# Kernel optimization log

Measured on AMD Instinct MI355X. Metric: run time of the kernel, lower is better.

The kernel has to match this reference:

```python
import jax, jax.numpy as jnp
import numpy as np

TOKENS = 512
IN_F = 8192
OUT_F = 8192
RANK = 64
NNZ = 8192
QMAX = 127.0  # int8 symmetric


def setup_inputs() -> dict:
    key = jax.random.key(0)
    ks = jax.random.split(key, 12)
    x = jax.random.normal(ks[0], (TOKENS, IN_F), dtype=jnp.float32)
    quantized_weight = jax.random.randint(ks[1], (OUT_F, IN_F), -128, 128, dtype=jnp.int32)
    weight_scale = jax.random.uniform(ks[2], (OUT_F,), minval=0.005, maxval=0.02, dtype=jnp.float32)
    smooth_scales = jax.random.uniform(ks[3], (IN_F,), minval=0.5, maxval=2.0, dtype=jnp.float32)
    act_scale = jnp.array([0.05], dtype=jnp.float32)
    outlier_rows = jax.random.randint(ks[4], (NNZ,), 0, OUT_F, dtype=jnp.int32)
    outlier_cols = jax.random.randint(ks[5], (NNZ,), 0, IN_F, dtype=jnp.int32)
    outlier_vals = jax.random.normal(ks[6], (NNZ,), dtype=jnp.float32) * 0.1
    svd_U = jax.random.normal(ks[7], (OUT_F, RANK), dtype=jnp.float32) * 0.02
    svd_S = jax.random.uniform(ks[8], (RANK,), minval=0.1, maxval=1.0, dtype=jnp.float32)
    svd_V = jax.random.normal(ks[9], (IN_F, RANK), dtype=jnp.float32) * 0.02
    bias = jax.random.normal(ks[10], (OUT_F,), dtype=jnp.float32) * 0.01
    return {"x": x, "quantized_weight": quantized_weight, "weight_scale": weight_scale,
            "smooth_scales": smooth_scales, "act_scale": act_scale,
            "outlier_rows": outlier_rows, "outlier_cols": outlier_cols,
            "outlier_vals": outlier_vals, "svd_U": svd_U, "svd_S": svd_S,
            "svd_V": svd_V, "bias": bias}


def reference(x, quantized_weight, weight_scale, smooth_scales, act_scale,
              outlier_rows, outlier_cols, outlier_vals, svd_U, svd_S, svd_V, bias):
    # SmoothQuant: migrate activation outliers into the weight scales
    x_s = x / smooth_scales  # [T, in]
    # per-tensor symmetric int8 activation fake-quant
    a = act_scale[0]
    x_q = jnp.clip(jnp.round(x_s / a), -QMAX - 1.0, QMAX)
    x_dq = x_q * a  # [T, in]
    # dequantize weight: per-output-channel scale, plus sparse outlier correction
    W = quantized_weight.astype(jnp.float32) * weight_scale[:, None]  # [out, in]
    W = W.at[outlier_rows, outlier_cols].add(outlier_vals)
    # dense quantized matmul
    y = x_dq @ W.T  # [T, out]
    # low-rank SVD residual: x @ (U S V^T)^T = ((x @ V) * S) @ U^T
    y = y + ((x_dq @ svd_V) * svd_S) @ svd_U.T
    return y + bias
```

## Files before the change

### kernel.cpp

```cpp
#include <hip/hip_runtime.h>
#include <hip/hip_bf16.h>

#define TOKENS 512
#define IN_F 8192
#define OUT_F 8192
#define RANK 64
#define NNZ 8192

#define KSPLIT 4
#define KRANGE (IN_F / KSPLIT)
#define BM 512
#define BN 64
#define BK 64
#define NT (KRANGE / BK)
#define LRSPLIT 16

typedef __attribute__((ext_vector_type(8))) short short8;
typedef __attribute__((ext_vector_type(4))) float f32x4;
typedef __attribute__((ext_vector_type(4))) int int4v;

__device__ __forceinline__ unsigned short f2bf(float f) {
  unsigned int u = __builtin_bit_cast(unsigned int, f);
  u += 0x7FFFu + ((u >> 16) & 1u);
  return (unsigned short)(u >> 16);
}
__device__ __forceinline__ float bf2f(unsigned short b) {
  unsigned int u = ((unsigned int)b) << 16;
  return __builtin_bit_cast(float, u);
}

__device__ __forceinline__ void gload_lds16(const void* g, void* l) {
  __builtin_amdgcn_global_load_lds(
      (const __attribute__((address_space(1))) unsigned int*)(g),
      (__attribute__((address_space(3))) unsigned int*)(l), 16, 0, 0);
}

#define WAIT_VM(n) asm volatile("s_waitcnt vmcnt(" #n ")" ::: "memory")
#define WAIT_LGKM0 asm volatile("s_waitcnt lgkmcnt(0)" ::: "memory")
#define SCHED0 __builtin_amdgcn_sched_barrier(0)

__global__ __launch_bounds__(256) void k_quant(const float* __restrict__ x,
                                               const float* __restrict__ smooth,
                                               const float* __restrict__ act,
                                               unsigned short* __restrict__ Abf,
                                               unsigned char* __restrict__ Aq) {
  int idx = blockIdx.x * 256 + threadIdx.x;
  int base = idx * 4;
  int col = base & (IN_F - 1);
  float a = act[0];
  float4 xx = *(const float4*)(x + base);
  float4 ss = *(const float4*)(smooth + col);
  float q0 = fminf(fmaxf(rintf((xx.x / ss.x) / a), -128.f), 127.f);
  float q1 = fminf(fmaxf(rintf((xx.y / ss.y) / a), -128.f), 127.f);
  float q2 = fminf(fmaxf(rintf((xx.z / ss.z) / a), -128.f), 127.f);
  float q3 = fminf(fmaxf(rintf((xx.w / ss.w) / a), -128.f), 127.f);
  ushort4 o;
  o.x = f2bf(q0); o.y = f2bf(q1); o.z = f2bf(q2); o.w = f2bf(q3);
  *(ushort4*)(Abf + base) = o;
  int i0 = (int)q0, i1 = (int)q1, i2 = (int)q2, i3 = (int)q3;
  unsigned int p = (i0 & 0xFF) | ((i1 & 0xFF) << 8) | ((i2 & 0xFF) << 16) |
                   ((unsigned)(i3 & 0xFF) << 24);
  *(unsigned int*)(Aq + base) = p;
}

__global__ __launch_bounds__(256) void k_lr1(const unsigned short* __restrict__ Abf,
                                             const float* __restrict__ V,
                                             const float* __restrict__ S,
                                             const float* __restrict__ act,
                                             float* __restrict__ t) {
  int bid = blockIdx.x;
  int mb = (bid & 3) * 128;
  int ksp = bid >> 2;
  int kb0 = ksp * 512;
  int tid = threadIdx.x, w = tid >> 6, l = tid & 63;
  int lr = l & 15, lg = l >> 4;
  f32x4 acc[2][4] = {};
  for (int ks = 0; ks < 16; ++ks) {
    int kb = kb0 + ks * 32;
    short8 af[2];
#pragma unroll
    for (int fi = 0; fi < 2; ++fi) {
      int row = mb + w * 32 + fi * 16 + lr;
      af[fi] = *(const short8*)(Abf + (size_t)row * IN_F + kb + lg * 8);
    }
    short8 bfr[4];
#pragma unroll
    for (int fj = 0; fj < 4; ++fj) {
      int rk = fj * 16 + lr;
      short8 bv;
#pragma unroll
      for (int j = 0; j < 8; ++j)
        bv[j] = (short)f2bf(V[(size_t)(kb + lg * 8 + j) * RANK + rk]);
      bfr[fj] = bv;
    }
#pragma unroll
    for (int fi = 0; fi < 2; ++fi)
#pragma unroll
      for (int fj = 0; fj < 4; ++fj)
        acc[fi][fj] = __builtin_amdgcn_mfma_f32_16x16x32_bf16(af[fi], bfr[fj], acc[fi][fj], 0, 0, 0);
  }
  float a = act[0];
  float* tk = t + (size_t)ksp * TOKENS * RANK;
#pragma unroll
  for (int fi = 0; fi < 2; ++fi)
#pragma unroll
    for (int fj = 0; fj < 4; ++fj) {
      int rk = fj * 16 + lr;
      float sc = a * S[rk];
#pragma unroll
      for (int r = 0; r < 4; ++r) {
        int tok = mb + w * 32 + fi * 16 + lg * 4 + r;
        tk[(size_t)tok * RANK + rk] = acc[fi][fj][r] * sc;
      }
    }
}

__global__ __launch_bounds__(256) void k_lr2(const float* __restrict__ t,
                                             const float* __restrict__ U,
                                             const float* __restrict__ bias,
                                             float* __restrict__ out) {
  int bid = blockIdx.x;
  int mb = (bid & 3) * 128;
  int nb = (bid >> 2) * 128;
  int tid = threadIdx.x, w = tid >> 6, l = tid & 63;
  int lr = l & 15, lg = l >> 4;
  int wm = w >> 1, wn = w & 1;
  f32x4 acc[4][4] = {};
#pragma unroll
  for (int kk = 0; kk < 2; ++kk) {
    short8 af[4], bfr[4];
#pragma unroll
    for (int fi = 0; fi < 4; ++fi) {
      int row = mb + wm * 64 + fi * 16 + lr;
      size_t off = (size_t)row * RANK + kk * 32 + lg * 8;
      float4 t0 = {0, 0, 0, 0}, t1 = {0, 0, 0, 0};
      for (int s = 0; s < LRSPLIT; ++s) {
        const float4* tp = (const float4*)(t + (size_t)s * TOKENS * RANK + off);
        float4 u0 = tp[0], u1 = tp[1];
        t0.x += u0.x; t0.y += u0.y; t0.z += u0.z; t0.w += u0.w;
        t1.x += u1.x; t1.y += u1.y; t1.z += u1.z; t1.w += u1.w;
      }
      af[fi][0] = f2bf(t0.x); af[fi][1] = f2bf(t0.y);
      af[fi][2] = f2bf(t0.z); af[fi][3] = f2bf(t0.w);
      af[fi][4] = f2bf(t1.x); af[fi][5] = f2bf(t1.y);
      af[fi][6] = f2bf(t1.z); af[fi][7] = f2bf(t1.w);
    }
#pragma unroll
    for (int fj = 0; fj < 4; ++fj) {
      int row = nb + wn * 64 + fj * 16 + lr;
      const float4* up = (const float4*)(U + (size_t)row * RANK + kk * 32 + lg * 8);
      float4 u0 = up[0], u1 = up[1];
      bfr[fj][0] = f2bf(u0.x); bfr[fj][1] = f2bf(u0.y);
      bfr[fj][2] = f2bf(u0.z); bfr[fj][3] = f2bf(u0.w);
      bfr[fj][4] = f2bf(u1.x); bfr[fj][5] = f2bf(u1.y);
      bfr[fj][6] = f2bf(u1.z); bfr[fj][7] = f2bf(u1.w);
    }
#pragma unroll
    for (int fi = 0; fi < 4; ++fi)
#pragma unroll
      for (int fj = 0; fj < 4; ++fj)
        acc[fi][fj] = __builtin_amdgcn_mfma_f32_16x16x32_bf16(af[fi], bfr[fj], acc[fi][fj], 0, 0, 0);
  }
#pragma unroll
  for (int fj = 0; fj < 4; ++fj) {
    int o = nb + wn * 64 + fj * 16 + lr;
    float b = bias[o];
#pragma unroll
    for (int fi = 0; fi < 4; ++fi)
#pragma unroll
      for (int r = 0; r < 4; ++r) {
        int tok = mb + wm * 64 + fi * 16 + lg * 4 + r;
        out[(size_t)tok * OUT_F + o] = b + acc[fi][fj][r];
      }
  }
}

__global__ __launch_bounds__(256) void k_outlier_merge(
    const unsigned short* __restrict__ Abf, const int* __restrict__ rows,
    const int* __restrict__ cols, const float* __restrict__ vals,
    const float* __restrict__ act, const float* __restrict__ wscale,
    const int* __restrict__ part, float* __restrict__ out) {
  __shared__ float accr[OUT_F];
  int tk = blockIdx.x;
  for (int i = threadIdx.x; i < OUT_F; i += 256) accr[i] = 0.f;
  __syncthreads();
  float a = act[0];
  for (int i = threadIdx.x; i < NNZ; i += 256) {
    int r = rows[i], c = cols[i];
    float v = vals[i];
    float xq = bf2f(Abf[(size_t)tk * IN_F + c]);
    atomicAdd(accr + r, a * xq * v);
  }
  __syncthreads();
  float* orow = out + (size_t)tk * OUT_F;
  const int* p0 = part + (size_t)tk * OUT_F;
  const int* p1 = p0 + (size_t)TOKENS * OUT_F;
  const int* p2 = p1 + (size_t)TOKENS * OUT_F;
  const int* p3 = p2 + (size_t)TOKENS * OUT_F;
  for (int i = threadIdx.x * 4; i < OUT_F; i += 1024) {
    int4v s0 = *(const int4v*)(p0 + i);
    int4v s1 = *(const int4v*)(p1 + i);
    int4v s2 = *(const int4v*)(p2 + i);
    int4v s3 = *(const int4v*)(p3 + i);
    float4 ws = *(const float4*)(wscale + i);
    float4 ov = *(const float4*)(orow + i);
    ov.x += accr[i + 0] + (float)(s0[0] + s1[0] + s2[0] + s3[0]) * a * ws.x;
    ov.y += accr[i + 1] + (float)(s0[1] + s1[1] + s2[1] + s3[1]) * a * ws.y;
    ov.z += accr[i + 2] + (float)(s0[2] + s1[2] + s2[2] + s3[2]) * a * ws.z;
    ov.w += accr[i + 3] + (float)(s0[3] + s1[3] + s2[3] + s3[3]) * a * ws.w;
    *(float4*)(orow + i) = ov;
  }
}

__global__ __launch_bounds__(512, 4) void k_gemm(const unsigned char* __restrict__ Aq,
                                                 const int* __restrict__ W,
                                                 int* __restrict__ part) {
  __shared__ __align__(16) unsigned char As[2][BM * BK];
  __shared__ __align__(16) unsigned char Bs[2][BN * BK];

  int d = blockIdx.x;
  int wg = (d & 7) * 64 + (d >> 3);
  int ks = wg >> 7;
  int nb = wg & 127;
  int kb0 = ks * KRANGE;

  int tid = threadIdx.x, w = tid >> 6, l = tid & 63;
  int lr = l & 15, lg = l >> 4;
  int wm = w >> 1, wn = w & 1;

  int4v acc[8][2] = {};
  int4v wa[2], wb[2];

  const int rW = tid >> 3;
  const int kcW = (tid & 7) * 8;
  const int uW = (kcW >> 4) ^ ((rW >> 1) & 3);
  const int offW = kcW & 15;

  auto LOAD_W = [&](int4v (&wr)[2], int kt) {
    const int* wp = W + (size_t)(nb * BN + rW) * IN_F + kb0 +
                    (kt & (NT - 1)) * BK + kcW;
    wr[0] = *(const int4v*)wp;
    wr[1] = *(const int4v*)(wp + 4);
  };
  auto STAGE_A = [&](int buf, int kt) {
    int kb = kb0 + (kt & (NT - 1)) * BK;
#pragma unroll
    for (int i = 0; i < 4; ++i) {
      int lidx = i * 512 + w * 64;
      int U = lidx + l;
      int r = U >> 2, up = U & 3;
      int u = up ^ ((r >> 1) & 3);
      gload_lds16(Aq + (size_t)r * IN_F + kb + u * 16, &As[buf][(size_t)lidx * 16]);
    }
  };
  auto DSWRITE_B = [&](int buf, const int4v (&wr)[2]) {
    unsigned int w0 = 0, w1 = 0;
#pragma unroll
    for (int j = 0; j < 4; ++j) w0 |= ((unsigned)(wr[0][j] & 0xFF)) << (8 * j);
#pragma unroll
    for (int j = 0; j < 4; ++j) w1 |= ((unsigned)(wr[1][j] & 0xFF)) << (8 * j);
    uint2 val; val.x = w0; val.y = w1;
    *(uint2*)(&Bs[buf][(size_t)rW * BK + uW * 16 + offW]) = val;
  };
  auto LDFA = [&](int buf, int row) -> int4v {
    int u = lg ^ ((row >> 1) & 3);
    return *(const int4v*)(&As[buf][(size_t)row * BK + u * 16]);
  };
  auto LDFB = [&](int buf, int row) -> int4v {
    int u = lg ^ ((row >> 1) & 3);
    return *(const int4v*)(&Bs[buf][(size_t)row * BK + u * 16]);
  };
  auto COMPUTE = [&](int buf) {
    int4v b0 = LDFB(buf, wn * 32 + lr);
    int4v b1 = LDFB(buf, wn * 32 + 16 + lr);
    __builtin_amdgcn_s_setprio(1);
#pragma unroll
    for (int fi = 0; fi < 8; ++fi) {
      int4v af = LDFA(buf, wm * 128 + fi * 16 + lr);
      acc[fi][0] = __builtin_amdgcn_mfma_i32_16x16x64_i8(af, b0, acc[fi][0], 0, 0, 0);
      acc[fi][1] = __builtin_amdgcn_mfma_i32_16x16x64_i8(af, b1, acc[fi][1], 0, 0, 0);
    }
    __builtin_amdgcn_s_setprio(0);
  };

  LOAD_W(wa, 0);
  STAGE_A(0, 0);
  WAIT_VM(4);
  DSWRITE_B(0, wa);
  LOAD_W(wa, 1);
  WAIT_VM(2);
  WAIT_LGKM0;
  SCHED0;
  __builtin_amdgcn_s_barrier();
  SCHED0;

#define ITER(kt, CUR, wcur, wnxt)                                   \
  {                                                                 \
    STAGE_A(CUR ^ 1, (kt) + 1);                                     \
    LOAD_W(wnxt, (kt) + 2);                                         \
    COMPUTE(CUR);                                                   \
    WAIT_VM(2);                                                     \
    DSWRITE_B(CUR ^ 1, wcur);                                       \
    WAIT_LGKM0;                                                     \
    SCHED0;                                                         \
    __builtin_amdgcn_s_barrier();                                   \
    SCHED0;                                                         \
  }

  for (int kt = 0; kt < NT; kt += 2) {
    ITER(kt, 0, wa, wb);
    ITER(kt + 1, 1, wb, wa);
  }
#undef ITER

  int* pp = part + (size_t)ks * TOKENS * OUT_F;
#pragma unroll
  for (int fj = 0; fj < 2; ++fj) {
    int o = nb * BN + wn * 32 + fj * 16 + lr;
#pragma unroll
    for (int fi = 0; fi < 8; ++fi)
#pragma unroll
      for (int rr = 0; rr < 4; ++rr) {
        int tok = wm * 128 + fi * 16 + lg * 4 + rr;
        pp[(size_t)tok * OUT_F + o] = acc[fi][fj][rr];
      }
  }
}

extern "C" void kernel_launch(void* const* d_in, const int* in_sizes, int n_in,
                              void* d_out, int out_size, void* d_ws, size_t ws_size,
                              hipStream_t stream) {
  const float* x = (const float*)d_in[0];
  const int* W = (const int*)d_in[1];
  const float* wscale = (const float*)d_in[2];
  const float* smooth = (const float*)d_in[3];
  const float* act = (const float*)d_in[4];
  const int* orow = (const int*)d_in[5];
  const int* ocol = (const int*)d_in[6];
  const float* oval = (const float*)d_in[7];
  const float* U = (const float*)d_in[8];
  const float* S = (const float*)d_in[9];
  const float* V = (const float*)d_in[10];
  const float* bias = (const float*)d_in[11];
  float* out = (float*)d_out;

  unsigned short* Abf = (unsigned short*)d_ws;
  unsigned char* Aq = (unsigned char*)d_ws + (size_t)TOKENS * IN_F * 2;
  float* t = (float*)((char*)d_ws + (size_t)TOKENS * IN_F * 3);
  int* part = (int*)((char*)d_ws + (size_t)TOKENS * IN_F * 3 +
                     (size_t)LRSPLIT * TOKENS * RANK * 4);

  k_quant<<<(TOKENS * IN_F / 4) / 256, 256, 0, stream>>>(x, smooth, act, Abf, Aq);
  k_gemm<<<512, 512, 0, stream>>>(Aq, W, part);
  k_lr1<<<64, 256, 0, stream>>>(Abf, V, S, act, t);
  k_lr2<<<256, 256, 0, stream>>>(t, U, bias, out);
  k_outlier_merge<<<TOKENS, 256, 0, stream>>>(Abf, orow, ocol, oval, act,
                                              wscale, part, out);
}
```

Baseline: 208.9 us.

## Rework int8 GEMM to 4 waves, BK=32, 16x16x32 MFMA, simpler pipeline

The int8 GEMM kernel now runs with 256 threads (4 waves) instead of 512. Each wave covers 128 token rows and all 64 output columns, using 8x4 accumulators. The K tile drops from 64 to 32 and the kernel switches to the 16x16x32 i8 MFMA with 8-byte LDS fragments. The hand-scheduled double-buffer macro is replaced by a plain loop with __syncthreads, and the explicit lgkm waits and sched barriers are removed. This trades fewer waves and more barriers per K for more register reuse of B fragments, which risks lower latency hiding and a slower MFMA variant.

```diff
diff --git a/kernel.cpp b/kernel.cpp
--- a/kernel.cpp
+++ b/kernel.cpp
@@ -11,7 +11,7 @@
 #define KRANGE (IN_F / KSPLIT)
 #define BM 512
 #define BN 64
-#define BK 64
+#define BK 32
 #define NT (KRANGE / BK)
 #define LRSPLIT 16
 
@@ -36,8 +36,6 @@
 }
 
 #define WAIT_VM(n) asm volatile("s_waitcnt vmcnt(" #n ")" ::: "memory")
-#define WAIT_LGKM0 asm volatile("s_waitcnt lgkmcnt(0)" ::: "memory")
-#define SCHED0 __builtin_amdgcn_sched_barrier(0)
 
 __global__ __launch_bounds__(256) void k_quant(const float* __restrict__ x,
                                                const float* __restrict__ smooth,
@@ -212,7 +210,7 @@
   }
 }
 
-__global__ __launch_bounds__(512, 4) void k_gemm(const unsigned char* __restrict__ Aq,
+__global__ __launch_bounds__(256, 3) void k_gemm(const unsigned char* __restrict__ Aq,
                                                  const int* __restrict__ W,
                                                  int* __restrict__ part) {
   __shared__ __align__(16) unsigned char As[2][BM * BK];
@@ -226,102 +224,94 @@
 
   int tid = threadIdx.x, w = tid >> 6, l = tid & 63;
   int lr = l & 15, lg = l >> 4;
-  int wm = w >> 1, wn = w & 1;
-
-  int4v acc[8][2] = {};
-  int4v wa[2], wb[2];
-
-  const int rW = tid >> 3;
-  const int kcW = (tid & 7) * 8;
-  const int uW = (kcW >> 4) ^ ((rW >> 1) & 3);
-  const int offW = kcW & 15;
-
-  auto LOAD_W = [&](int4v (&wr)[2], int kt) {
-    const int* wp = W + (size_t)(nb * BN + rW) * IN_F + kb0 +
-                    (kt & (NT - 1)) * BK + kcW;
+
+  int4v acc[8][4] = {};
+  int4v wr[2];
+
+  const int rW = tid >> 2;
+  const int kcW = (tid & 3) * 8;
+  const int uW = (kcW >> 4) ^ ((rW >> 1) & 1);
+  const int hW = (kcW >> 3) & 1;
+
+  auto LOAD_W = [&](int kt) {
+    const int* wp = W + (size_t)(nb * BN + rW) * IN_F + kb0 + kt * BK + kcW;
     wr[0] = *(const int4v*)wp;
     wr[1] = *(const int4v*)(wp + 4);
   };
   auto STAGE_A = [&](int buf, int kt) {
-    int kb = kb0 + (kt & (NT - 1)) * BK;
+    int kb = kb0 + kt * BK;
 #pragma unroll
     for (int i = 0; i < 4; ++i) {
-      int lidx = i * 512 + w * 64;
-      int U = lidx + l;
-      int r = U >> 2, up = U & 3;
-      int u = up ^ ((r >> 1) & 3);
-      gload_lds16(Aq + (size_t)r * IN_F + kb + u * 16, &As[buf][(size_t)lidx * 16]);
-    }
-  };
-  auto DSWRITE_B = [&](int buf, const int4v (&wr)[2]) {
+      int base = i * 256 + w * 64;
+      int idx = base + l;
+      int r = idx >> 1, u = idx & 1;
+      int us = u ^ ((r >> 1) & 1);
+      gload_lds16(Aq + (size_t)r * IN_F + kb + us * 16,
+                  &As[buf][(size_t)base * 16]);
+    }
+  };
+  auto WRITE_B = [&](int buf) {
     unsigned int w0 = 0, w1 = 0;
 #pragma unroll
     for (int j = 0; j < 4; ++j) w0 |= ((unsigned)(wr[0][j] & 0xFF)) << (8 * j);
 #pragma unroll
     for (int j = 0; j < 4; ++j) w1 |= ((unsigned)(wr[1][j] & 0xFF)) << (8 * j);
     uint2 val; val.x = w0; val.y = w1;
-    *(uint2*)(&Bs[buf][(size_t)rW * BK + uW * 16 + offW]) = val;
-  };
-  auto LDFA = [&](int buf, int row) -> int4v {
-    int u = lg ^ ((row >> 1) & 3);
-    return *(const int4v*)(&As[buf][(size_t)row * BK + u * 16]);
-  };
-  auto LDFB = [&](int buf, int row) -> int4v {
-    int u = lg ^ ((row >> 1) & 3);
-    return *(const int4v*)(&Bs[buf][(size_t)row * BK + u * 16]);
+    *(uint2*)(&Bs[buf][(size_t)rW * BK + uW * 16 + hW * 8]) = val;
+  };
+  auto LDFA = [&](int buf, int row) -> long {
+    int u = (lg >> 1) ^ ((row >> 1) & 1);
+    return *(const long*)(&As[buf][(size_t)row * BK + u * 16 + (lg & 1) * 8]);
+  };
+  auto LDFB = [&](int buf, int row) -> long {
+    int u = (lg >> 1) ^ ((row >> 1) & 1);
+    return *(const long*)(&Bs[buf][(size_t)row * BK + u * 16 + (lg & 1) * 8]);
   };
   auto COMPUTE = [&](int buf) {
-    int4v b0 = LDFB(buf, wn * 32 + lr);
-    int4v b1 = LDFB(buf, wn * 32 + 16 + lr);
+    long bfrag[4];
+#pragma unroll
+    for (int fj = 0; fj < 4; ++fj) bfrag[fj] = LDFB(buf, fj * 16 + lr);
     __builtin_amdgcn_s_setprio(1);
 #pragma unroll
     for (int fi = 0; fi < 8; ++fi) {
-      int4v af = LDFA(buf, wm * 128 + fi * 16 + lr);
-      acc[fi][0] = __builtin_amdgcn_mfma_i32_16x16x64_i8(af, b0, acc[fi][0], 0, 0, 0);
-      acc[fi][1] = __builtin_amdgcn_mfma_i32_16x16x64_i8(af, b1, acc[fi][1], 0, 0, 0);
+      long af = LDFA(buf, w * 128 + fi * 16 + lr);
+#pragma unroll
+      for (int fj = 0; fj < 4; ++fj)
+        acc[fi][fj] = __builtin_amdgcn_mfma_i32_16x16x32_i8(af, bfrag[fj],
+                                                            acc[fi][fj], 0, 0, 0);
     }
     __builtin_amdgcn_s_setprio(0);
   };
 
-  LOAD_W(wa, 0);
+  LOAD_W(0);
   STAGE_A(0, 0);
   WAIT_VM(4);
-  DSWRITE_B(0, wa);
-  LOAD_W(wa, 1);
-  WAIT_VM(2);
-  WAIT_LGKM0;
-  SCHED0;
-  __builtin_amdgcn_s_barrier();
-  SCHED0;
-
-#define ITER(kt, CUR, wcur, wnxt)                                   \
-  {                                                                 \
-    STAGE_A(CUR ^ 1, (kt) + 1);                                     \
-    LOAD_W(wnxt, (kt) + 2);                                         \
-    COMPUTE(CUR);                                                   \
-    WAIT_VM(2);                                                     \
-    DSWRITE_B(CUR ^ 1, wcur);                                       \
-    WAIT_LGKM0;                                                     \
-    SCHED0;                                                         \
-    __builtin_amdgcn_s_barrier();                                   \
-    SCHED0;                                                         \
-  }
-
-  for (int kt = 0; kt < NT; kt += 2) {
-    ITER(kt, 0, wa, wb);
-    ITER(kt + 1, 1, wb, wa);
-  }
-#undef ITER
+  WRITE_B(0);
+  __syncthreads();
+
+  for (int kt = 0; kt < NT; ++kt) {
+    int cur = kt & 1;
+    if (kt + 1 < NT) {
+      LOAD_W(kt + 1);
+      STAGE_A(cur ^ 1, kt + 1);
+    }
+    COMPUTE(cur);
+    if (kt + 1 < NT) {
+      WAIT_VM(4);
+      WRITE_B(cur ^ 1);
+    }
+    __syncthreads();
+  }
 
   int* pp = part + (size_t)ks * TOKENS * OUT_F;
 #pragma unroll
-  for (int fj = 0; fj < 2; ++fj) {
-    int o = nb * BN + wn * 32 + fj * 16 + lr;
+  for (int fj = 0; fj < 4; ++fj) {
+    int o = nb * BN + fj * 16 + lr;
 #pragma unroll
     for (int fi = 0; fi < 8; ++fi)
 #pragma unroll
       for (int rr = 0; rr < 4; ++rr) {
-        int tok = wm * 128 + fi * 16 + lg * 4 + rr;
+        int tok = w * 128 + fi * 16 + lg * 4 + rr;
         pp[(size_t)tok * OUT_F + o] = acc[fi][fj][rr];
       }
   }
@@ -351,7 +341,7 @@
                      (size_t)LRSPLIT * TOKENS * RANK * 4);
 
   k_quant<<<(TOKENS * IN_F / 4) / 256, 256, 0, stream>>>(x, smooth, act, Abf, Aq);
-  k_gemm<<<512, 512, 0, stream>>>(Aq, W, part);
+  k_gemm<<<512, 256, 0, stream>>>(Aq, W, part);
   k_lr1<<<64, 256, 0, stream>>>(Abf, V, S, act, t);
   k_lr2<<<256, 256, 0, stream>>>(t, U, bias, out);
   k_outlier_merge<<<TOKENS, 256, 0, stream>>>(Abf, orow, ocol, oval, act,
```

Result: slower. 249.0 us (+19.2%).
